# Optimization experiments

Measured on AMD Instinct MI355X. Metric: run time of the kernel, lower is better.

The kernel has to match this reference:

```python
import jax, jax.numpy as jnp
import numpy as np

# SCVC config: groups=8, kernel_share=True, kernel_size=3, out_channels=128
N, G, OG, DX, DY = 8, 8, 16, 256, 256  # OG = out_channels // groups


def setup_inputs() -> dict:
    key = jax.random.key(0)
    k = jax.random.split(key, 5)
    return {
        "x": jax.random.normal(k[0], (N, G, DX), dtype=jnp.float32),
        "y": jax.random.normal(k[1], (N, G, DY), dtype=jnp.float32),
        # kernel_C per group: (OG, 1) -> stacked (G, OG); init normal * 3/sqrt(1)
        "C": jax.random.normal(k[2], (G, OG), dtype=jnp.float32) * 3.0,
        # RandomConv1d weights (out=OG, in=1, k=2) per group: stacked (G, OG, 2)
        "wA": jax.random.normal(k[3], (G, OG, 2), dtype=jnp.float32) * 3.0,
        "wB": jax.random.normal(k[4], (G, OG, 2), dtype=jnp.float32) * 3.0,
    }


def _shifted(v):
    # v: (N, G, D). Returns (v[..., p-1], v[..., p+1]) with zero boundaries,
    # which is exactly what pad->dilated conv(k=2, dil=2)->center split computes.
    left = jnp.pad(v, ((0, 0), (0, 0), (1, 0)))[..., :-1]
    right = jnp.pad(v, ((0, 0), (0, 0), (0, 1)))[..., 1:]
    return left, right


def reference(x, y, C, wA, wB):
    # Per-group SCVC (kernel_share=True, 1 channel per group), concat over groups.
    # cross[n,g,o,p,q] = C[g,o] * x[n,g,p] * y[n,g,q]  (batch_cross_product)
    cross = jnp.einsum('go,ngp,ngq->ngopq', C, x, y)
    # dilated-conv correction: a[n,g,o,p] = wA0*x[p-1] + wA1*x[p+1]
    xl, xr = _shifted(x)
    yl, yr = _shifted(y)
    a = (wA[None, :, :, 0, None] * xl[:, :, None, :]
         + wA[None, :, :, 1, None] * xr[:, :, None, :])  # (N, G, OG, DX)
    b = (wB[None, :, :, 0, None] * yl[:, :, None, :]
         + wB[None, :, :, 1, None] * yr[:, :, None, :])  # (N, G, OG, DY)
    out = cross + a[..., :, None] + b[..., None, :]       # (N, G, OG, DX, DY)
    return out.reshape(N, G * OG, DX, DY)
```

## Files before the change

### kernel.cpp

```cpp
#include <hip/hip_runtime.h>


#define N_  8
#define G_  8
#define OG_ 16
#define DX_ 256
#define DY_ 256

typedef float vfloat4 __attribute__((ext_vector_type(4)));

__global__ __launch_bounds__(256) void scvc_kernel(
    const float* __restrict__ x,
    const float* __restrict__ y,
    const float* __restrict__ C,
    const float* __restrict__ wA,
    const float* __restrict__ wB,
    float* __restrict__ out)
{
    __shared__ float sarr[DX_];
    __shared__ float aarr[DX_];
    __shared__ float ybuf[DY_];
    __shared__ float bbuf[DY_];

    const int tid = threadIdx.x;
    const int qv  = tid & 63;
    const int wv  = tid >> 6;

    for (int j = 0; j < 4; ++j) {
        const int t  = (blockIdx.x << 2) | j;
        const int go = t & 127;
        const int ng = ((t >> 7) << 3) | (go >> 4);

        __syncthreads();
        {
            const float  co = C[go];
            const float2 wa = ((const float2*)wA)[go];
            const float2 wb = ((const float2*)wB)[go];
            const float* xrow = x + ng * DX_;
            const float* yrow = y + ng * DY_;

            float xv = xrow[tid];
            float xl = (tid > 0)       ? xrow[tid - 1] : 0.0f;
            float xr = (tid < DX_ - 1) ? xrow[tid + 1] : 0.0f;
            sarr[tid] = co * xv;
            aarr[tid] = fmaf(wa.x, xl, wa.y * xr);

            float yv = yrow[tid];
            float yl = (tid > 0)       ? yrow[tid - 1] : 0.0f;
            float yr = (tid < DY_ - 1) ? yrow[tid + 1] : 0.0f;
            ybuf[tid] = yv;
            bbuf[tid] = fmaf(wb.x, yl, wb.y * yr);
        }
        __syncthreads();

        const vfloat4 y4 = ((const vfloat4*)ybuf)[qv];
        const vfloat4 b4 = ((const vfloat4*)bbuf)[qv];

        float* obase = out + (size_t)t * (DX_ * DY_) + (size_t)(wv * 64) * DY_;

#pragma unroll 8
        for (int i = 0; i < 64; ++i) {
            const int p  = (wv << 6) + i;
            const float s  = sarr[p];
            const float av = aarr[p];
            vfloat4 v;
            v.x = fmaf(s, y4.x, av + b4.x);
            v.y = fmaf(s, y4.y, av + b4.y);
            v.z = fmaf(s, y4.z, av + b4.z);
            v.w = fmaf(s, y4.w, av + b4.w);
            ((vfloat4*)(obase + (size_t)i * DY_))[qv] = v;
        }
    }
}

extern "C" void kernel_launch(void* const* d_in, const int* in_sizes, int n_in,
                              void* d_out, int out_size, void* d_ws, size_t ws_size,
                              hipStream_t stream) {
    const float* x  = (const float*)d_in[0];
    const float* y  = (const float*)d_in[1];
    const float* C  = (const float*)d_in[2];
    const float* wA = (const float*)d_in[3];
    const float* wB = (const float*)d_in[4];
    float* out = (float*)d_out;

    const int nblocks = 256;
    scvc_kernel<<<nblocks, 256, 0, stream>>>(x, y, C, wA, wB, out);
}
```

Baseline: 260.0 us.

## Split into precompute pass and flat grid-stride streaming kernel with fallback

After: 263.2 us. About the same (+1.3%).

```diff
diff --git a/kernel.cpp b/kernel.cpp
--- a/kernel.cpp
+++ b/kernel.cpp
@@ -9,67 +9,123 @@
 
 typedef float vfloat4 __attribute__((ext_vector_type(4)));
 
-__global__ __launch_bounds__(256) void scvc_kernel(
-    const float* __restrict__ x,
+__global__ __launch_bounds__(256) void scvc_precompute(
+    const float* __restrict__ x, const float* __restrict__ y,
+    const float* __restrict__ C, const float* __restrict__ wA,
+    const float* __restrict__ wB,
+    float* __restrict__ sw, float* __restrict__ aw, float* __restrict__ bw)
+{
+    const int t  = blockIdx.x;
+    const int i  = threadIdx.x;
+    const int go = t & 127;
+    const int ng = ((t >> 7) << 3) | (go >> 4);
+
+    const float  co = C[go];
+    const float2 wa = ((const float2*)wA)[go];
+    const float2 wb = ((const float2*)wB)[go];
+
+    const float* xrow = x + ng * DX_;
+    const float* yrow = y + ng * DY_;
+
+    const float xv = xrow[i];
+    const float xl = (i > 0)       ? xrow[i - 1] : 0.0f;
+    const float xr = (i < DX_ - 1) ? xrow[i + 1] : 0.0f;
+    sw[t * DX_ + i] = co * xv;
+    aw[t * DX_ + i] = fmaf(wa.x, xl, wa.y * xr);
+
+    const float yl = (i > 0)       ? yrow[i - 1] : 0.0f;
+    const float yr = (i < DY_ - 1) ? yrow[i + 1] : 0.0f;
+    bw[t * DY_ + i] = fmaf(wb.x, yl, wb.y * yr);
+}
+
+__global__ __launch_bounds__(256) void scvc_stream(
+    const float* __restrict__ sw,
+    const float* __restrict__ aw,
+    const float* __restrict__ bw,
     const float* __restrict__ y,
-    const float* __restrict__ C,
-    const float* __restrict__ wA,
-    const float* __restrict__ wB,
     float* __restrict__ out)
+{
+    const int gid = blockIdx.x * 256 + threadIdx.x;
+    vfloat4* out4 = (vfloat4*)out;
+    const vfloat4* bw4 = (const vfloat4*)bw;
+    const vfloat4* y4p = (const vfloat4*)y;
+
+#pragma unroll 4
+    for (int it = 0; it < 256; ++it) {
+        const int idx = it * 65536 + gid;
+        const int rp = idx >> 6;
+        const int qv = idx & 63;
+        const int t  = idx >> 14;
+        const int ng = idx >> 18;
+
+        const float   s  = sw[rp];
+        const float   av = aw[rp];
+        const vfloat4 b4 = bw4[(t  << 6) | qv];
+        const vfloat4 yy = y4p[(ng << 6) | qv];
+
+        vfloat4 v;
+        v.x = fmaf(s, yy.x, av + b4.x);
+        v.y = fmaf(s, yy.y, av + b4.y);
+        v.z = fmaf(s, yy.z, av + b4.z);
+        v.w = fmaf(s, yy.w, av + b4.w);
+        out4[idx] = v;
+    }
+}
+
+__global__ __launch_bounds__(256) void scvc_kernel_r4(
+    const float* __restrict__ x, const float* __restrict__ y,
+    const float* __restrict__ C, const float* __restrict__ wA,
+    const float* __restrict__ wB, float* __restrict__ out)
 {
     __shared__ float sarr[DX_];
     __shared__ float aarr[DX_];
     __shared__ float ybuf[DY_];
     __shared__ float bbuf[DY_];
 
-    const int tid = threadIdx.x;
-    const int qv  = tid & 63;
-    const int wv  = tid >> 6;
+    const int t    = blockIdx.x >> 1;
+    const int half = blockIdx.x & 1;
+    const int go   = t & 127;
+    const int ng   = ((t >> 7) << 3) | (go >> 4);
+    const int tid  = threadIdx.x;
 
-    for (int j = 0; j < 4; ++j) {
-        const int t  = (blockIdx.x << 2) | j;
-        const int go = t & 127;
-        const int ng = ((t >> 7) << 3) | (go >> 4);
+    const float  co = C[go];
+    const float2 wa = ((const float2*)wA)[go];
+    const float2 wb = ((const float2*)wB)[go];
 
-        __syncthreads();
-        {
-            const float  co = C[go];
-            const float2 wa = ((const float2*)wA)[go];
-            const float2 wb = ((const float2*)wB)[go];
-            const float* xrow = x + ng * DX_;
-            const float* yrow = y + ng * DY_;
+    const float* xrow = x + ng * DX_;
+    const float* yrow = y + ng * DY_;
+    {
+        float xv = xrow[tid];
+        float xl = (tid > 0)       ? xrow[tid - 1] : 0.0f;
+        float xr = (tid < DX_ - 1) ? xrow[tid + 1] : 0.0f;
+        sarr[tid] = co * xv;
+        aarr[tid] = fmaf(wa.x, xl, wa.y * xr);
+        float yv = yrow[tid];
+        float yl = (tid > 0)       ? yrow[tid - 1] : 0.0f;
+        float yr = (tid < DY_ - 1) ? yrow[tid + 1] : 0.0f;
+        ybuf[tid] = yv;
+        bbuf[tid] = fmaf(wb.x, yl, wb.y * yr);
+    }
+    __syncthreads();
 
-            float xv = xrow[tid];
-            float xl = (tid > 0)       ? xrow[tid - 1] : 0.0f;
-            float xr = (tid < DX_ - 1) ? xrow[tid + 1] : 0.0f;
-            sarr[tid] = co * xv;
-            aarr[tid] = fmaf(wa.x, xl, wa.y * xr);
+    const int qv = tid & 63;
+    const int wv = tid >> 6;
+    const int p0 = half * (DX_ / 2) + wv * 32;
+    const vfloat4 y4 = ((const vfloat4*)ybuf)[qv];
+    const vfloat4 b4 = ((const vfloat4*)bbuf)[qv];
+    float* obase = out + (size_t)t * (DX_ * DY_) + (size_t)p0 * DY_;
 
-            float yv = yrow[tid];
-            float yl = (tid > 0)       ? yrow[tid - 1] : 0.0f;
-            float yr = (tid < DY_ - 1) ? yrow[tid + 1] : 0.0f;
-            ybuf[tid] = yv;
-            bbuf[tid] = fmaf(wb.x, yl, wb.y * yr);
-        }
-        __syncthreads();
-
-        const vfloat4 y4 = ((const vfloat4*)ybuf)[qv];
-        const vfloat4 b4 = ((const vfloat4*)bbuf)[qv];
-
-        float* obase = out + (size_t)t * (DX_ * DY_) + (size_t)(wv * 64) * DY_;
-
-#pragma unroll 8
-        for (int i = 0; i < 64; ++i) {
-            const int p  = (wv << 6) + i;
-            const float s  = sarr[p];
-            const float av = aarr[p];
-            vfloat4 v;
-            v.x = fmaf(s, y4.x, av + b4.x);
-            v.y = fmaf(s, y4.y, av + b4.y);
-            v.z = fmaf(s, y4.z, av + b4.z);
-            v.w = fmaf(s, y4.w, av + b4.w);
-            ((vfloat4*)(obase + (size_t)i * DY_))[qv] = v;
-        }
+#pragma unroll 4
+    for (int i = 0; i < 32; ++i) {
+        const int p  = p0 + i;
+        const float s  = sarr[p];
+        const float av = aarr[p];
+        vfloat4 v;
+        v.x = fmaf(s, y4.x, av + b4.x);
+        v.y = fmaf(s, y4.y, av + b4.y);
+        v.z = fmaf(s, y4.z, av + b4.z);
+        v.w = fmaf(s, y4.w, av + b4.w);
+        ((vfloat4*)(obase + (size_t)i * DY_))[qv] = v;
     }
 }
 
@@ -83,6 +139,19 @@
     const float* wB = (const float*)d_in[4];
     float* out = (float*)d_out;
 
-    const int nblocks = 256;
-    scvc_kernel<<<nblocks, 256, 0, stream>>>(x, y, C, wA, wB, out);
+    const size_t nchan = (size_t)N_ * G_ * OG_;
+    const size_t arr   = nchan * DX_;
+    const size_t need  = 3 * arr * sizeof(float);
+
+    if (ws_size >= need && d_ws != nullptr) {
+        float* sw = (float*)d_ws;
+        float* aw = sw + arr;
+        float* bw = aw + arr;
+        scvc_precompute<<<(int)nchan, 256, 0, stream>>>(x, y, C, wA, wB,
+                                                        sw, aw, bw);
+        scvc_stream<<<256, 256, 0, stream>>>(sw, aw, bw, y, out);
+    } else {
+        scvc_kernel_r4<<<N_ * G_ * OG_ * 2, 256, 0, stream>>>(x, y, C, wA, wB,
+                                                              out);
+    }
 }
```
